# Performance work log

Measured on AMD Instinct MI355X. Metric: run time of the kernel, lower is better.

## Reference

```python
import jax, jax.numpy as jnp
import numpy as np

T, B, E, H, O = 128, 512, 256, 1024, 256


def setup_inputs() -> dict:
    key = jax.random.key(0)
    ks = jax.random.split(key, 7)
    s = lambda k, shape, fan: jax.random.normal(k, shape, jnp.float32) / np.sqrt(fan)
    return {
        "seq": jax.random.normal(ks[0], (T, B, E), jnp.float32),
        "Wh_w": s(ks[1], (H, H), H),
        "Wh_b": s(ks[2], (H,), H),
        "Wi_w": s(ks[3], (H, E), E),
        "Wi_b": s(ks[4], (H,), E),
        "Wo_w": s(ks[5], (O, H), H),
        "Wo_b": s(ks[6], (O,), H),
    }


def reference(seq, Wh_w, Wh_b, Wi_w, Wi_b, Wo_w, Wo_b):
    # Elman RNN: h_t = tanh(Wh h_{t-1} + Wi x_t); returns o_T = Wo h_T.
    Bsz = seq.shape[1]
    h0 = jnp.zeros((Bsz, Wh_w.shape[0]), seq.dtype)
    # Precompute input projections for all steps in one big GEMM: [T,B,H]
    xi = jnp.einsum('tbe,he->tbh', seq, Wi_w) + Wi_b + Wh_b

    def step(h, xt):
        h = jnp.tanh(h @ Wh_w.T + xt)
        return h, None

    hT, _ = jax.lax.scan(step, h0, xi)
    return hT @ Wo_w.T + Wo_b
```

## Files before the change

kernel.cpp:

```cpp
#include <hip/hip_runtime.h>
#include <hip/hip_bf16.h>


#define T_ 128
#define B_ 512
#define E_ 256
#define H_ 1024
#define O_ 256
#define RG 16
#define HB (B_ * H_)
#define ROWB 2064

typedef __bf16 bf16x8 __attribute__((ext_vector_type(8)));
typedef float  f32x4  __attribute__((ext_vector_type(4)));
typedef unsigned int u32x2 __attribute__((ext_vector_type(2)));
typedef unsigned int u32x4 __attribute__((ext_vector_type(4)));

static __device__ __forceinline__ unsigned short f2bf(float f) {
  unsigned u = __float_as_uint(f);
  u += 0x7fff + ((u >> 16) & 1);
  return (unsigned short)(u >> 16);
}
static __device__ __forceinline__ unsigned pk2(float a, float b) {
  return (unsigned)f2bf(a) | ((unsigned)f2bf(b) << 16);
}
static __device__ __forceinline__ bf16x8 cvt8(const float* p) {
  float4 f0 = reinterpret_cast<const float4*>(p)[0];
  float4 f1 = reinterpret_cast<const float4*>(p)[1];
  union { u32x4 u; bf16x8 v; } r;
  r.u = (u32x4){pk2(f0.x, f0.y), pk2(f0.z, f0.w), pk2(f1.x, f1.y), pk2(f1.z, f1.w)};
  return r.v;
}
static __device__ __forceinline__ float fast_tanh(float x) {
  float e = __builtin_amdgcn_exp2f(x * 2.8853900817779268f);
  return 1.f - 2.f / (e + 1.f);
}

static __device__ __forceinline__ void poll1(const unsigned* fl, unsigned tgt) {
  for (;;) {
    unsigned a;
    asm volatile("global_load_dword %0, %1, off sc0 sc1"
                 : "=v"(a) : "v"(fl) : "memory");
    asm volatile("s_waitcnt vmcnt(0)" ::: "memory");
    __builtin_amdgcn_sched_barrier(0);
    if (a >= tgt) return;
    __builtin_amdgcn_s_sleep(1);
  }
}

__global__ void prep_kernel(const float* __restrict__ seq,
                            unsigned short* __restrict__ seq_bf,
                            unsigned* __restrict__ flags) {
  size_t idx = (size_t)blockIdx.x * blockDim.x + threadIdx.x;
  size_t stride = (size_t)gridDim.x * blockDim.x;
  const size_t nchunk = (size_t)T_ * B_ * E_ / 8;
  for (size_t i = idx; i < nchunk; i += stride) {
    union { bf16x8 v; u32x4 u; } r;
    r.v = cvt8(seq + i * 8);
    *reinterpret_cast<u32x4*>(seq_bf + i * 8) = r.u;
  }
  if (idx < 1024) {
    unsigned z = 0;
    asm volatile("global_store_dword %0, %1, off sc0 sc1"
                 :: "v"(flags + idx), "v"(z) : "memory");
  }
}

__global__ __launch_bounds__(512, 2) void rnn_fused(
    const unsigned short* __restrict__ seq_bf, const float* __restrict__ Wh_w,
    const float* __restrict__ Wh_b, const float* __restrict__ Wi_w,
    const float* __restrict__ Wi_b, const float* __restrict__ Wo_w,
    const float* __restrict__ Wo_b,
    unsigned short* __restrict__ hbuf, unsigned* __restrict__ flags,
    float* __restrict__ out) {
  __shared__ __align__(16) unsigned char As[RG * ROWB];
  __shared__ __align__(16) float red[8][RG][132];

  const int tid = threadIdx.x;
  const int bid = blockIdx.x;
  const int g = bid & 31, p = bid >> 5;
  const int R0 = g * RG, C0 = p * 128;
  const int lane = tid & 63, wv = tid >> 6;
  const int l15 = lane & 15, k4 = lane >> 4;
  const int srow = lane >> 2, scc = lane & 3;

  bf16x8 bh[8][4];
#pragma unroll
  for (int nn = 0; nn < 8; ++nn) {
    const float* wp = Wh_w + (size_t)(C0 + nn * 16 + l15) * H_ + wv * 128 + k4 * 8;
#pragma unroll
    for (int ks = 0; ks < 4; ++ks) bh[nn][ks] = cvt8(wp + ks * 32);
  }
  bf16x8 wif[8];
#pragma unroll
  for (int nn = 0; nn < 8; ++nn)
    wif[nn] = cvt8(Wi_w + (size_t)(C0 + nn * 16 + l15) * E_ + wv * 32 + k4 * 8);

  const int erow = tid >> 5, ec = (tid & 31) * 4;
  f32x4 bias4;
  {
    f32x4 b1 = *reinterpret_cast<const f32x4*>(Wh_b + C0 + ec);
    f32x4 b2 = *reinterpret_cast<const f32x4*>(Wi_b + C0 + ec);
    bias4 = b1 + b2;
  }
  const unsigned* wvfl = flags + g * 32 + wv;
  unsigned* myfl = flags + g * 32 + p;
  const size_t hoff_b = ((size_t)(R0 + erow) * H_ + C0 + ec) * 2;

  for (int t = 0; t < T_; ++t) {
    f32x4 acc[8];
#pragma unroll
    for (int nn = 0; nn < 8; ++nn) acc[nn] = (f32x4){0.f, 0.f, 0.f, 0.f};
    bf16x8 xa = *reinterpret_cast<const bf16x8*>(
        seq_bf + ((size_t)t * B_ + R0 + l15) * E_ + wv * 32 + k4 * 8);
    u32x4 s0, s1, s2, s3;
    if (t > 0) {
      poll1(wvfl, (unsigned)t);
      const unsigned char* hb =
          (const unsigned char*)(hbuf + (size_t)((t - 1) & 1) * HB) +
          (size_t)R0 * 2048 + wv * 256;
#define RNN_LD(J, SV)                                                            \
      asm volatile("global_load_dwordx4 %0, %1, off sc0 sc1"                     \
                   : "=v"(SV)                                                    \
                   : "v"(hb + (size_t)srow * 2048 + ((J) * 4 + scc) * 16)        \
                   : "memory");
      RNN_LD(0, s0) RNN_LD(1, s1) RNN_LD(2, s2) RNN_LD(3, s3)
#undef RNN_LD
    }
#pragma unroll
    for (int nn = 0; nn < 8; ++nn)
      acc[nn] = __builtin_amdgcn_mfma_f32_16x16x32_bf16(xa, wif[nn], acc[nn], 0, 0, 0);
    if (t > 0) {
      asm volatile("s_waitcnt vmcnt(0)" ::: "memory");
      __builtin_amdgcn_sched_barrier(0);
#define RNN_ST(J, SV)                                                            \
      *reinterpret_cast<u32x4*>(                                                 \
          &As[srow * ROWB + (wv * 16 + (J) * 4 + scc) * 16]) = SV;
      RNN_ST(0, s0) RNN_ST(1, s1) RNN_ST(2, s2) RNN_ST(3, s3)
#undef RNN_ST
      asm volatile("s_waitcnt lgkmcnt(0)" ::: "memory");
      __builtin_amdgcn_sched_barrier(0);
#pragma unroll
      for (int ks = 0; ks < 4; ++ks) {
        bf16x8 a = *reinterpret_cast<const bf16x8*>(
            &As[l15 * ROWB + (wv * 16 + ks * 4 + k4) * 16]);
#pragma unroll
        for (int nn = 0; nn < 8; ++nn)
          acc[nn] = __builtin_amdgcn_mfma_f32_16x16x32_bf16(a, bh[nn][ks], acc[nn], 0, 0, 0);
      }
    }
#pragma unroll
    for (int nn = 0; nn < 8; ++nn)
#pragma unroll
      for (int r = 0; r < 4; ++r)
        red[wv][k4 * 4 + r][nn * 16 + l15] = acc[nn][r];
    __syncthreads();
    {
      f32x4 v = *reinterpret_cast<const f32x4*>(&red[0][erow][ec]);
#pragma unroll
      for (int s = 1; s < 8; ++s)
        v += *reinterpret_cast<const f32x4*>(&red[s][erow][ec]);
      v += bias4;
      u32x2 pv = {pk2(fast_tanh(v[0]), fast_tanh(v[1])),
                  pk2(fast_tanh(v[2]), fast_tanh(v[3]))};
      const unsigned char* dst =
          (const unsigned char*)hbuf + (size_t)(t & 1) * (HB * 2) + hoff_b;
      asm volatile("global_store_dwordx2 %0, %1, off sc0 sc1"
                   :: "v"(dst), "v"(pv) : "memory");
    }
    asm volatile("s_waitcnt vmcnt(0)" ::: "memory");
    __syncthreads();
    if (tid == 0) {
      unsigned fv = (unsigned)(t + 1);
      asm volatile("global_store_dword %0, %1, off sc0 sc1"
                   :: "v"(myfl), "v"(fv) : "memory");
    }
  }

  if (p >= 2) return;
  {
    poll1(wvfl, (unsigned)T_);
    const unsigned char* hb =
        (const unsigned char*)(hbuf + (size_t)((T_ - 1) & 1) * HB) +
        (size_t)R0 * 2048 + wv * 256;
    u32x4 s0, s1, s2, s3;
#define RNN_LD(J, SV)                                                            \
    asm volatile("global_load_dwordx4 %0, %1, off sc0 sc1"                       \
                 : "=v"(SV)                                                      \
                 : "v"(hb + (size_t)srow * 2048 + ((J) * 4 + scc) * 16)          \
                 : "memory");
    RNN_LD(0, s0) RNN_LD(1, s1) RNN_LD(2, s2) RNN_LD(3, s3)
#undef RNN_LD
    asm volatile("s_waitcnt vmcnt(0)" ::: "memory");
    __builtin_amdgcn_sched_barrier(0);
#define RNN_ST(J, SV)                                                            \
    *reinterpret_cast<u32x4*>(                                                   \
        &As[srow * ROWB + (wv * 16 + (J) * 4 + scc) * 16]) = SV;
    RNN_ST(0, s0) RNN_ST(1, s1) RNN_ST(2, s2) RNN_ST(3, s3)
#undef RNN_ST
    asm volatile("s_waitcnt lgkmcnt(0)" ::: "memory");
    __builtin_amdgcn_sched_barrier(0);
    f32x4 acc[8];
#pragma unroll
    for (int nn = 0; nn < 8; ++nn) acc[nn] = (f32x4){0.f, 0.f, 0.f, 0.f};
#pragma unroll
    for (int ks = 0; ks < 4; ++ks) {
      bf16x8 a = *reinterpret_cast<const bf16x8*>(
          &As[l15 * ROWB + (wv * 16 + ks * 4 + k4) * 16]);
#pragma unroll
      for (int nn = 0; nn < 8; ++nn) {
        bf16x8 b = cvt8(Wo_w + (size_t)(C0 + nn * 16 + l15) * H_ +
                        wv * 128 + ks * 32 + k4 * 8);
        acc[nn] = __builtin_amdgcn_mfma_f32_16x16x32_bf16(a, b, acc[nn], 0, 0, 0);
      }
    }
#pragma unroll
    for (int nn = 0; nn < 8; ++nn)
#pragma unroll
      for (int r = 0; r < 4; ++r)
        red[wv][k4 * 4 + r][nn * 16 + l15] = acc[nn][r];
    __syncthreads();
    {
      f32x4 v = *reinterpret_cast<const f32x4*>(&red[0][erow][ec]);
#pragma unroll
      for (int s = 1; s < 8; ++s)
        v += *reinterpret_cast<const f32x4*>(&red[s][erow][ec]);
      v += *reinterpret_cast<const f32x4*>(Wo_b + C0 + ec);
      *reinterpret_cast<f32x4*>(out + (size_t)(R0 + erow) * O_ + C0 + ec) = v;
    }
  }
}

extern "C" void kernel_launch(void* const* d_in, const int* in_sizes, int n_in,
                              void* d_out, int out_size, void* d_ws, size_t ws_size,
                              hipStream_t stream) {
  const float* seq  = (const float*)d_in[0];
  const float* Wh_w = (const float*)d_in[1];
  const float* Wh_b = (const float*)d_in[2];
  const float* Wi_w = (const float*)d_in[3];
  const float* Wi_b = (const float*)d_in[4];
  const float* Wo_w = (const float*)d_in[5];
  const float* Wo_b = (const float*)d_in[6];

  char* ws = (char*)d_ws;
  unsigned short* hbuf   = (unsigned short*)ws; ws += (size_t)2 * HB * 2;
  unsigned*       flags  = (unsigned*)ws;       ws += 4096;
  unsigned short* seq_bf = (unsigned short*)ws;

  prep_kernel<<<2048, 256, 0, stream>>>(seq, seq_bf, flags);
  rnn_fused<<<256, 512, 0, stream>>>(seq_bf, Wh_w, Wh_b, Wi_w, Wi_b, Wo_w, Wo_b,
                                     hbuf, flags, (float*)d_out);
}
```

Baseline: 453.3 us.

## Use per-wave flags, direct global A-fragment loads, and double-buffered reduction

Each wave now publishes its own completion flag and consumers poll the eight wave flags of a producer block, which removes the second block-wide barrier per timestep. The hidden-state A fragments are loaded straight from global memory in MFMA layout rather than staged through an LDS tile, and the reduction buffer is double-buffered by timestep parity so the next step's writes cannot race with the current step's reads. The cost is wider flag polling and possibly less coalesced global loads for the A fragments.

```diff
diff --git a/kernel.cpp b/kernel.cpp
--- a/kernel.cpp
+++ b/kernel.cpp
@@ -9,7 +9,6 @@
 #define O_ 256
 #define RG 16
 #define HB (B_ * H_)
-#define ROWB 2064
 
 typedef __bf16 bf16x8 __attribute__((ext_vector_type(8)));
 typedef float  f32x4  __attribute__((ext_vector_type(4)));
@@ -36,14 +35,16 @@
   return 1.f - 2.f / (e + 1.f);
 }
 
-static __device__ __forceinline__ void poll1(const unsigned* fl, unsigned tgt) {
+static __device__ __forceinline__ void poll8(const unsigned* fl, unsigned tgt) {
   for (;;) {
-    unsigned a;
-    asm volatile("global_load_dword %0, %1, off sc0 sc1"
-                 : "=v"(a) : "v"(fl) : "memory");
+    u32x4 a, b;
+    asm volatile("global_load_dwordx4 %0, %1, off sc0 sc1" : "=v"(a) : "v"(fl) : "memory");
+    asm volatile("global_load_dwordx4 %0, %1, off sc0 sc1" : "=v"(b) : "v"(fl + 4) : "memory");
     asm volatile("s_waitcnt vmcnt(0)" ::: "memory");
     __builtin_amdgcn_sched_barrier(0);
-    if (a >= tgt) return;
+    unsigned m = min(min(min(a.x, a.y), min(a.z, a.w)),
+                     min(min(b.x, b.y), min(b.z, b.w)));
+    if (m >= tgt) return;
     __builtin_amdgcn_s_sleep(1);
   }
 }
@@ -59,7 +60,7 @@
     r.v = cvt8(seq + i * 8);
     *reinterpret_cast<u32x4*>(seq_bf + i * 8) = r.u;
   }
-  if (idx < 1024) {
+  if (idx < 2048) {
     unsigned z = 0;
     asm volatile("global_store_dword %0, %1, off sc0 sc1"
                  :: "v"(flags + idx), "v"(z) : "memory");
@@ -73,8 +74,7 @@
     const float* __restrict__ Wo_b,
     unsigned short* __restrict__ hbuf, unsigned* __restrict__ flags,
     float* __restrict__ out) {
-  __shared__ __align__(16) unsigned char As[RG * ROWB];
-  __shared__ __align__(16) float red[8][RG][132];
+  __shared__ __align__(16) float red[2][8][RG][132];
 
   const int tid = threadIdx.x;
   const int bid = blockIdx.x;
@@ -82,7 +82,6 @@
   const int R0 = g * RG, C0 = p * 128;
   const int lane = tid & 63, wv = tid >> 6;
   const int l15 = lane & 15, k4 = lane >> 4;
-  const int srow = lane >> 2, scc = lane & 3;
 
   bf16x8 bh[8][4];
 #pragma unroll
@@ -96,16 +95,18 @@
   for (int nn = 0; nn < 8; ++nn)
     wif[nn] = cvt8(Wi_w + (size_t)(C0 + nn * 16 + l15) * E_ + wv * 32 + k4 * 8);
 
-  const int erow = tid >> 5, ec = (tid & 31) * 4;
+  const int er = lane >> 2;
+  const int ecl = wv * 16 + (lane & 3) * 4;
   f32x4 bias4;
   {
-    f32x4 b1 = *reinterpret_cast<const f32x4*>(Wh_b + C0 + ec);
-    f32x4 b2 = *reinterpret_cast<const f32x4*>(Wi_b + C0 + ec);
+    f32x4 b1 = *reinterpret_cast<const f32x4*>(Wh_b + C0 + ecl);
+    f32x4 b2 = *reinterpret_cast<const f32x4*>(Wi_b + C0 + ecl);
     bias4 = b1 + b2;
   }
-  const unsigned* wvfl = flags + g * 32 + wv;
-  unsigned* myfl = flags + g * 32 + p;
-  const size_t hoff_b = ((size_t)(R0 + erow) * H_ + C0 + ec) * 2;
+  const unsigned* wvfl = flags + g * 64 + wv * 8;
+  unsigned* myfl = flags + g * 64 + p * 8 + wv;
+  const size_t hoff_b = ((size_t)(R0 + er) * H_ + C0 + ecl) * 2;
+  const size_t afr_e = (size_t)(R0 + l15) * H_ + wv * 128 + k4 * 8;
 
   for (int t = 0; t < T_; ++t) {
     f32x4 acc[8];
@@ -113,19 +114,19 @@
     for (int nn = 0; nn < 8; ++nn) acc[nn] = (f32x4){0.f, 0.f, 0.f, 0.f};
     bf16x8 xa = *reinterpret_cast<const bf16x8*>(
         seq_bf + ((size_t)t * B_ + R0 + l15) * E_ + wv * 32 + k4 * 8);
-    u32x4 s0, s1, s2, s3;
+    u32x4 a0, a1, a2, a3;
     if (t > 0) {
-      poll1(wvfl, (unsigned)t);
-      const unsigned char* hb =
-          (const unsigned char*)(hbuf + (size_t)((t - 1) & 1) * HB) +
-          (size_t)R0 * 2048 + wv * 256;
-#define RNN_LD(J, SV)                                                            \
-      asm volatile("global_load_dwordx4 %0, %1, off sc0 sc1"                     \
-                   : "=v"(SV)                                                    \
-                   : "v"(hb + (size_t)srow * 2048 + ((J) * 4 + scc) * 16)        \
-                   : "memory");
-      RNN_LD(0, s0) RNN_LD(1, s1) RNN_LD(2, s2) RNN_LD(3, s3)
-#undef RNN_LD
+      poll8(wvfl, (unsigned)t);
+      const unsigned char* ab =
+          (const unsigned char*)(hbuf + (size_t)((t - 1) & 1) * HB + afr_e);
+      asm volatile("global_load_dwordx4 %0, %1, off sc0 sc1"
+                   : "=v"(a0) : "v"(ab) : "memory");
+      asm volatile("global_load_dwordx4 %0, %1, off sc0 sc1"
+                   : "=v"(a1) : "v"(ab + 64) : "memory");
+      asm volatile("global_load_dwordx4 %0, %1, off sc0 sc1"
+                   : "=v"(a2) : "v"(ab + 128) : "memory");
+      asm volatile("global_load_dwordx4 %0, %1, off sc0 sc1"
+                   : "=v"(a3) : "v"(ab + 192) : "memory");
     }
 #pragma unroll
     for (int nn = 0; nn < 8; ++nn)
@@ -133,33 +134,31 @@
     if (t > 0) {
       asm volatile("s_waitcnt vmcnt(0)" ::: "memory");
       __builtin_amdgcn_sched_barrier(0);
-#define RNN_ST(J, SV)                                                            \
-      *reinterpret_cast<u32x4*>(                                                 \
-          &As[srow * ROWB + (wv * 16 + (J) * 4 + scc) * 16]) = SV;
-      RNN_ST(0, s0) RNN_ST(1, s1) RNN_ST(2, s2) RNN_ST(3, s3)
-#undef RNN_ST
-      asm volatile("s_waitcnt lgkmcnt(0)" ::: "memory");
-      __builtin_amdgcn_sched_barrier(0);
-#pragma unroll
-      for (int ks = 0; ks < 4; ++ks) {
-        bf16x8 a = *reinterpret_cast<const bf16x8*>(
-            &As[l15 * ROWB + (wv * 16 + ks * 4 + k4) * 16]);
-#pragma unroll
-        for (int nn = 0; nn < 8; ++nn)
-          acc[nn] = __builtin_amdgcn_mfma_f32_16x16x32_bf16(a, bh[nn][ks], acc[nn], 0, 0, 0);
-      }
-    }
-#pragma unroll
-    for (int nn = 0; nn < 8; ++nn)
-#pragma unroll
-      for (int r = 0; r < 4; ++r)
-        red[wv][k4 * 4 + r][nn * 16 + l15] = acc[nn][r];
+      union { u32x4 u; bf16x8 v; } af;
+#define RNN_HMF(KS, AV)                                                          \
+      af.u = AV;                                                                 \
+      _Pragma("unroll")                                                          \
+      for (int nn = 0; nn < 8; ++nn)                                             \
+        acc[nn] = __builtin_amdgcn_mfma_f32_16x16x32_bf16(af.v, bh[nn][KS],      \
+                                                          acc[nn], 0, 0, 0);
+      RNN_HMF(0, a0) RNN_HMF(1, a1) RNN_HMF(2, a2) RNN_HMF(3, a3)
+#undef RNN_HMF
+    }
+    {
+      float* rb = &red[t & 1][wv][0][0];
+#pragma unroll
+      for (int nn = 0; nn < 8; ++nn)
+#pragma unroll
+        for (int r = 0; r < 4; ++r)
+          rb[(k4 * 4 + r) * 132 + nn * 16 + l15] = acc[nn][r];
+    }
     __syncthreads();
     {
-      f32x4 v = *reinterpret_cast<const f32x4*>(&red[0][erow][ec]);
+      const float* rb = &red[t & 1][0][0][0];
+      f32x4 v = *reinterpret_cast<const f32x4*>(rb + er * 132 + ecl);
 #pragma unroll
       for (int s = 1; s < 8; ++s)
-        v += *reinterpret_cast<const f32x4*>(&red[s][erow][ec]);
+        v += *reinterpret_cast<const f32x4*>(rb + (s * RG + er) * 132 + ecl);
       v += bias4;
       u32x2 pv = {pk2(fast_tanh(v[0]), fast_tanh(v[1])),
                   pk2(fast_tanh(v[2]), fast_tanh(v[3]))};
@@ -169,8 +168,7 @@
                    :: "v"(dst), "v"(pv) : "memory");
     }
     asm volatile("s_waitcnt vmcnt(0)" ::: "memory");
-    __syncthreads();
-    if (tid == 0) {
+    if (lane == 0) {
       unsigned fv = (unsigned)(t + 1);
       asm volatile("global_store_dword %0, %1, off sc0 sc1"
                    :: "v"(myfl), "v"(fv) : "memory");
@@ -179,54 +177,47 @@
 
   if (p >= 2) return;
   {
-    poll1(wvfl, (unsigned)T_);
-    const unsigned char* hb =
-        (const unsigned char*)(hbuf + (size_t)((T_ - 1) & 1) * HB) +
-        (size_t)R0 * 2048 + wv * 256;
-    u32x4 s0, s1, s2, s3;
-#define RNN_LD(J, SV)                                                            \
-    asm volatile("global_load_dwordx4 %0, %1, off sc0 sc1"                       \
-                 : "=v"(SV)                                                      \
-                 : "v"(hb + (size_t)srow * 2048 + ((J) * 4 + scc) * 16)          \
-                 : "memory");
-    RNN_LD(0, s0) RNN_LD(1, s1) RNN_LD(2, s2) RNN_LD(3, s3)
-#undef RNN_LD
+    poll8(wvfl, (unsigned)T_);
+    const unsigned char* ab =
+        (const unsigned char*)(hbuf + (size_t)((T_ - 1) & 1) * HB + afr_e);
+    u32x4 a0, a1, a2, a3;
+    asm volatile("global_load_dwordx4 %0, %1, off sc0 sc1" : "=v"(a0) : "v"(ab) : "memory");
+    asm volatile("global_load_dwordx4 %0, %1, off sc0 sc1" : "=v"(a1) : "v"(ab + 64) : "memory");
+    asm volatile("global_load_dwordx4 %0, %1, off sc0 sc1" : "=v"(a2) : "v"(ab + 128) : "memory");
+    asm volatile("global_load_dwordx4 %0, %1, off sc0 sc1" : "=v"(a3) : "v"(ab + 192) : "memory");
     asm volatile("s_waitcnt vmcnt(0)" ::: "memory");
     __builtin_amdgcn_sched_barrier(0);
-#define RNN_ST(J, SV)                                                            \
-    *reinterpret_cast<u32x4*>(                                                   \
-        &As[srow * ROWB + (wv * 16 + (J) * 4 + scc) * 16]) = SV;
-    RNN_ST(0, s0) RNN_ST(1, s1) RNN_ST(2, s2) RNN_ST(3, s3)
-#undef RNN_ST
-    asm volatile("s_waitcnt lgkmcnt(0)" ::: "memory");
-    __builtin_amdgcn_sched_barrier(0);
     f32x4 acc[8];
 #pragma unroll
     for (int nn = 0; nn < 8; ++nn) acc[nn] = (f32x4){0.f, 0.f, 0.f, 0.f};
-#pragma unroll
-    for (int ks = 0; ks < 4; ++ks) {
-      bf16x8 a = *reinterpret_cast<const bf16x8*>(
-          &As[l15 * ROWB + (wv * 16 + ks * 4 + k4) * 16]);
-#pragma unroll
-      for (int nn = 0; nn < 8; ++nn) {
-        bf16x8 b = cvt8(Wo_w + (size_t)(C0 + nn * 16 + l15) * H_ +
-                        wv * 128 + ks * 32 + k4 * 8);
-        acc[nn] = __builtin_amdgcn_mfma_f32_16x16x32_bf16(a, b, acc[nn], 0, 0, 0);
-      }
-    }
-#pragma unroll
-    for (int nn = 0; nn < 8; ++nn)
-#pragma unroll
-      for (int r = 0; r < 4; ++r)
-        red[wv][k4 * 4 + r][nn * 16 + l15] = acc[nn][r];
+    union { u32x4 u; bf16x8 v; } af;
+#define RNN_OMF(KS, AV)                                                          \
+    af.u = AV;                                                                   \
+    _Pragma("unroll")                                                            \
+    for (int nn = 0; nn < 8; ++nn) {                                             \
+      bf16x8 b = cvt8(Wo_w + (size_t)(C0 + nn * 16 + l15) * H_ +                 \
+                      wv * 128 + (KS) * 32 + k4 * 8);                            \
+      acc[nn] = __builtin_amdgcn_mfma_f32_16x16x32_bf16(af.v, b, acc[nn], 0, 0, 0); \
+    }
+    RNN_OMF(0, a0) RNN_OMF(1, a1) RNN_OMF(2, a2) RNN_OMF(3, a3)
+#undef RNN_OMF
+    {
+      float* rb = &red[0][wv][0][0];
+#pragma unroll
+      for (int nn = 0; nn < 8; ++nn)
+#pragma unroll
+        for (int r = 0; r < 4; ++r)
+          rb[(k4 * 4 + r) * 132 + nn * 16 + l15] = acc[nn][r];
+    }
     __syncthreads();
     {
-      f32x4 v = *reinterpret_cast<const f32x4*>(&red[0][erow][ec]);
+      const float* rb = &red[0][0][0][0];
+      f32x4 v = *reinterpret_cast<const f32x4*>(rb + er * 132 + ecl);
 #pragma unroll
       for (int s = 1; s < 8; ++s)
-        v += *reinterpret_cast<const f32x4*>(&red[s][erow][ec]);
-      v += *reinterpret_cast<const f32x4*>(Wo_b + C0 + ec);
-      *reinterpret_cast<f32x4*>(out + (size_t)(R0 + erow) * O_ + C0 + ec) = v;
+        v += *reinterpret_cast<const f32x4*>(rb + (s * RG + er) * 132 + ecl);
+      v += *reinterpret_cast<const f32x4*>(Wo_b + C0 + ecl);
+      *reinterpret_cast<f32x4*>(out + (size_t)(R0 + er) * O_ + C0 + ecl) = v;
     }
   }
 }
@@ -244,7 +235,7 @@
 
   char* ws = (char*)d_ws;
   unsigned short* hbuf   = (unsigned short*)ws; ws += (size_t)2 * HB * 2;
-  unsigned*       flags  = (unsigned*)ws;       ws += 4096;
+  unsigned*       flags  = (unsigned*)ws;       ws += 8192;
   unsigned short* seq_bf = (unsigned short*)ws;
 
   prep_kernel<<<2048, 256, 0, stream>>>(seq, seq_bf, flags);
```

New measurement: 1.079 ms. 2.38x slower.
